# Kernel tuning notes

Hardware: AMD Instinct MI355X
Metric: run time of the kernel (lower is better)

Reference implementation:

```python
import jax, jax.numpy as jnp
import numpy as np

B, T, N_EMBED, HEAD_SIZE = 8, 2048, 1024, 64


def setup_inputs() -> dict:
    key = jax.random.key(0)
    kx, kq, kk, kv = jax.random.split(key, 4)
    x = jax.random.normal(kx, (B, T, N_EMBED), dtype=jnp.float32)
    # nn.Linear(n_embed, head_size, bias=False) -> weight [head_size, n_embed];
    # we store the transposed [n_embed, head_size] so projection is x @ W.
    s = 1.0 / np.sqrt(N_EMBED)
    Wq = jax.random.normal(kq, (N_EMBED, HEAD_SIZE), dtype=jnp.float32) * s
    Wk = jax.random.normal(kk, (N_EMBED, HEAD_SIZE), dtype=jnp.float32) * s
    Wv = jax.random.normal(kv, (N_EMBED, HEAD_SIZE), dtype=jnp.float32) * s
    pad_mask = jnp.ones((B, T), dtype=jnp.int32)
    return {"x": x, "pad_mask": pad_mask, "Wq": Wq, "Wk": Wk, "Wv": Wv}


def reference(x, pad_mask, Wq, Wk, Wv):
    Bq, Tq, C = x.shape  # C == n_embed
    q = x @ Wq  # [B,T,H]
    k = x @ Wk  # self-attention path (enc_x is None)
    v = x @ Wv
    # NOTE: original divides by C**0.5 with C = n_embed, not head_size.
    scores = jnp.einsum("bth,bsh->bts", q, k) / jnp.sqrt(jnp.asarray(C, x.dtype))
    causal = jnp.tril(jnp.ones((Tq, Tq), dtype=bool))  # tril[:T,:T] != 0
    keep = causal[None, :, :] & (pad_mask[:, None, :] != 0)  # [B,T,T]
    scores = jnp.where(keep, scores, -jnp.inf)
    attn = jax.nn.softmax(scores, axis=-1)
    return jnp.einsum("bts,bsh->bth", attn, v)  # [B,T,head_size]
```

## Files before the change

kernel.cpp:

```cpp
#include <hip/hip_runtime.h>

#define DEV static __device__ __forceinline__

typedef float f32x4 __attribute__((ext_vector_type(4)));
typedef __bf16 bf16x8 __attribute__((ext_vector_type(8)));
typedef unsigned short u16x8 __attribute__((ext_vector_type(8)));

#define MFMA(a, b, c) __builtin_amdgcn_mfma_f32_16x16x32_bf16((a), (b), (c), 0, 0, 0)

#define TT 2048
#define CE 1024
#define HS 64

#define WBT_E 0
#define Q_E   196608
#define K_E   (Q_E + 1048576)
#define VT_E  (K_E + 1048576)

DEV unsigned short cvt_bf16(float f) {
    unsigned int u = __builtin_bit_cast(unsigned int, f);
    u += 0x7FFFu + ((u >> 16) & 1u);
    return (unsigned short)(u >> 16);
}

DEV bf16x8 ld_bf8(const unsigned short* p) {
    union { u16x8 u; bf16x8 b; } v;
    v.u = *(const u16x8*)p;
    return v.b;
}

__global__ __launch_bounds__(256) void wconv_kernel(
        const float* __restrict__ Wq, const float* __restrict__ Wk,
        const float* __restrict__ Wv, unsigned short* __restrict__ wbt) {
    __shared__ unsigned short Tr[64 * 72];
    const int blk = blockIdx.x;
    const int head = blk >> 4, kt = blk & 15;
    const int k0 = kt * 64;
    const float* W = (head == 0) ? Wq : ((head == 1) ? Wk : Wv);
    const float sc = (head == 0) ? 0.045084220027780106f : 1.0f;
    const int t = threadIdx.x;
    const int rrow = t >> 4, c4 = (t & 15) * 4;
    for (int i = 0; i < 4; ++i) {
        int krow = rrow + i * 16;
        f32x4 f = *(const f32x4*)(W + (size_t)(k0 + krow) * 64 + c4);
        Tr[(c4 + 0) * 72 + krow] = cvt_bf16(f[0] * sc);
        Tr[(c4 + 1) * 72 + krow] = cvt_bf16(f[1] * sc);
        Tr[(c4 + 2) * 72 + krow] = cvt_bf16(f[2] * sc);
        Tr[(c4 + 3) * 72 + krow] = cvt_bf16(f[3] * sc);
    }
    __syncthreads();
    const int n = t >> 2, off = (t & 3) * 16;
    u16x8 a0 = *(const u16x8*)&Tr[n * 72 + off];
    u16x8 a1 = *(const u16x8*)&Tr[n * 72 + off + 8];
    unsigned short* dst = wbt + head * 65536 + n * 1024 + k0 + off;
    *(u16x8*)dst = a0;
    *(u16x8*)(dst + 8) = a1;
}

__global__ __launch_bounds__(256) void proj_kernel(
        const float* __restrict__ x, const unsigned short* __restrict__ wbt,
        unsigned short* __restrict__ qws, unsigned short* __restrict__ kws,
        unsigned short* __restrict__ vtws) {
    __shared__ __align__(16) unsigned short As[2 * 32 * 72];
    __shared__ __align__(16) unsigned short Ws[2 * 192 * 72];

    const int t = threadIdx.x;
    const int lane = t & 63, w = t >> 6;
    const int quad = lane >> 4, c = lane & 15;
    const int t0 = blockIdx.x * 32;
    const int xrow = t >> 3, xc = (t & 7) * 8;

    f32x4 acc[2][3] = {};

    {
        f32x4 f0 = *(const f32x4*)(x + (size_t)(t0 + xrow) * CE + xc);
        f32x4 f1 = *(const f32x4*)(x + (size_t)(t0 + xrow) * CE + xc + 4);
        u16x8 pk;
        for (int j = 0; j < 4; ++j) { pk[j] = cvt_bf16(f0[j]); pk[4 + j] = cvt_bf16(f1[j]); }
        *(u16x8*)&As[xrow * 72 + xc] = pk;
        for (int i = 0; i < 6; ++i) {
            int id = t + 256 * i, n = id >> 3, cc = id & 7;
            *(u16x8*)&Ws[n * 72 + cc * 8] = *(const u16x8*)(wbt + n * 1024 + cc * 8);
        }
    }
    __syncthreads();

    for (int step = 0; step < 16; ++step) {
        const int pb = step & 1, nb = pb ^ 1;
        const int ksn = ((step + 1) & 15) * 64;
        f32x4 f0 = *(const f32x4*)(x + (size_t)(t0 + xrow) * CE + ksn + xc);
        f32x4 f1 = *(const f32x4*)(x + (size_t)(t0 + xrow) * CE + ksn + xc + 4);
        u16x8 wv[6];
        for (int i = 0; i < 6; ++i) {
            int id = t + 256 * i, n = id >> 3, cc = id & 7;
            wv[i] = *(const u16x8*)(wbt + n * 1024 + ksn + cc * 8);
        }
        for (int kk = 0; kk < 2; ++kk) {
            bf16x8 a0 = ld_bf8(&As[pb * 2304 + c * 72 + kk * 32 + quad * 8]);
            bf16x8 a1 = ld_bf8(&As[pb * 2304 + (16 + c) * 72 + kk * 32 + quad * 8]);
            for (int nt = 0; nt < 3; ++nt) {
                bf16x8 bb = ld_bf8(&Ws[pb * 13824 + (w * 48 + nt * 16 + c) * 72 + kk * 32 + quad * 8]);
                acc[0][nt] = MFMA(a0, bb, acc[0][nt]);
                acc[1][nt] = MFMA(a1, bb, acc[1][nt]);
            }
        }
        {
            u16x8 pk;
            for (int j = 0; j < 4; ++j) { pk[j] = cvt_bf16(f0[j]); pk[4 + j] = cvt_bf16(f1[j]); }
            *(u16x8*)&As[nb * 2304 + xrow * 72 + xc] = pk;
            for (int i = 0; i < 6; ++i) {
                int id = t + 256 * i, n = id >> 3, cc = id & 7;
                *(u16x8*)&Ws[nb * 13824 + n * 72 + cc * 8] = wv[i];
            }
        }
        __syncthreads();
    }

    unsigned short* TT2 = As;
    for (int mt = 0; mt < 2; ++mt)
        for (int nt = 0; nt < 3; ++nt) {
            f32x4 a = acc[mt][nt];
            int col = w * 48 + nt * 16 + c;
            for (int r = 0; r < 4; ++r) {
                int row = mt * 16 + quad * 4 + r;
                size_t tg = (size_t)(t0 + row);
                unsigned short hv = cvt_bf16(a[r]);
                if (col < 64)       qws[tg * HS + col] = hv;
                else if (col < 128) kws[tg * HS + col - 64] = hv;
                else                TT2[(col - 128) * 48 + row] = hv;
            }
        }
    __syncthreads();
    {
        int h = t >> 2, off = (t & 3) * 8;
        u16x8 v = *(const u16x8*)&TT2[h * 48 + off];
        int b = t0 >> 11, tl0 = t0 & 2047;
        *(u16x8*)(vtws + (size_t)(b * 64 + h) * TT + tl0 + off) = v;
    }
}

__global__ __launch_bounds__(256) void flash_kernel(
        const unsigned short* __restrict__ qws, const unsigned short* __restrict__ kws,
        const unsigned short* __restrict__ vtws, const int* __restrict__ pmask,
        float* __restrict__ out) {
    __shared__ __align__(16) unsigned short Ks[2 * 64 * 72];
    __shared__ __align__(16) unsigned short Vts[2 * 64 * 72];
    __shared__ int pms[2 * 64];

    const int t = threadIdx.x, blk = blockIdx.x;
    const int b = blk >> 5, qi = blk & 31;
    const int t0 = qi * 64;
    const int lane = t & 63, w = t >> 6;
    const int quad = lane >> 4, c = lane & 15;
    const float NEGINF = -__builtin_inff();

    const int krow0 = t >> 3, kcc = (t & 7) * 8;
    const int vrow0 = w * 16 + (lane >> 3), vcc = (lane & 7) * 8;

    bf16x8 qf[2];
    for (int kk = 0; kk < 2; ++kk)
        qf[kk] = ld_bf8(qws + (size_t)(b * TT + t0 + w * 16 + c) * HS + kk * 32 + quad * 8);

    u16x8 kr0 = *(const u16x8*)(kws + (size_t)(b * TT + krow0) * HS + kcc);
    u16x8 kr1 = *(const u16x8*)(kws + (size_t)(b * TT + krow0 + 32) * HS + kcc);
    u16x8 vr0 = *(const u16x8*)(vtws + (size_t)(b * 64 + vrow0) * TT + vcc);
    u16x8 vr1 = *(const u16x8*)(vtws + (size_t)(b * 64 + vrow0 + 8) * TT + vcc);
    int pr = (t < 64) ? pmask[b * TT + t] : 0;
    *(u16x8*)&Ks[krow0 * 72 + kcc] = kr0;
    *(u16x8*)&Ks[(krow0 + 32) * 72 + kcc] = kr1;
    *(u16x8*)&Vts[vrow0 * 72 + vcc] = vr0;
    *(u16x8*)&Vts[(vrow0 + 8) * 72 + vcc] = vr1;
    if (t < 64) pms[t] = pr;
    __syncthreads();

    f32x4 o[4] = {};
    float m_run[4], l_run[4];
    for (int r = 0; r < 4; ++r) { m_run[r] = NEGINF; l_run[r] = 0.0f; }

    for (int jj = 0; jj <= qi; ++jj) {
        const int pb = jj & 1, nb = pb ^ 1;
        const int jn = (jj < qi) ? jj + 1 : qi;
        kr0 = *(const u16x8*)(kws + (size_t)(b * TT + jn * 64 + krow0) * HS + kcc);
        kr1 = *(const u16x8*)(kws + (size_t)(b * TT + jn * 64 + krow0 + 32) * HS + kcc);
        vr0 = *(const u16x8*)(vtws + (size_t)(b * 64 + vrow0) * TT + jn * 64 + vcc);
        vr1 = *(const u16x8*)(vtws + (size_t)(b * 64 + vrow0 + 8) * TT + jn * 64 + vcc);
        pr = (t < 64) ? pmask[b * TT + jn * 64 + t] : 0;

        f32x4 s4[4] = {};
        for (int kk = 0; kk < 2; ++kk)
            for (int nt = 0; nt < 4; ++nt) {
                bf16x8 bb = ld_bf8(&Ks[pb * 4608 + (nt * 16 + c) * 72 + kk * 32 + quad * 8]);
                s4[nt] = MFMA(qf[kk], bb, s4[nt]);
            }

        int pm4[4];
        for (int nt = 0; nt < 4; ++nt) pm4[nt] = pms[pb * 64 + nt * 16 + c];
        if (jj == qi) {
            for (int nt = 0; nt < 4; ++nt) {
                int col = nt * 16 + c;
                for (int r = 0; r < 4; ++r) {
                    int rowl = w * 16 + quad * 4 + r;
                    if (pm4[nt] == 0 || col > rowl) s4[nt][r] = NEGINF;
                }
            }
        } else {
            for (int nt = 0; nt < 4; ++nt)
                if (pm4[nt] == 0)
                    for (int r = 0; r < 4; ++r) s4[nt][r] = NEGINF;
        }

        float al[4];
        for (int r = 0; r < 4; ++r) {
            float mx = fmaxf(fmaxf(s4[0][r], s4[1][r]), fmaxf(s4[2][r], s4[3][r]));
            mx = fmaxf(mx, __shfl_xor(mx, 1, 64));
            mx = fmaxf(mx, __shfl_xor(mx, 2, 64));
            mx = fmaxf(mx, __shfl_xor(mx, 4, 64));
            mx = fmaxf(mx, __shfl_xor(mx, 8, 64));
            float mnew = fmaxf(m_run[r], mx);
            al[r] = (mnew == NEGINF) ? 1.0f : exp2f(m_run[r] - mnew);
            m_run[r] = mnew;
        }
        for (int nt = 0; nt < 4; ++nt)
            for (int r = 0; r < 4; ++r)
                s4[nt][r] = (s4[nt][r] == NEGINF) ? 0.0f : exp2f(s4[nt][r] - m_run[r]);
        for (int r = 0; r < 4; ++r) {
            float rs = s4[0][r] + s4[1][r] + s4[2][r] + s4[3][r];
            rs += __shfl_xor(rs, 1, 64);
            rs += __shfl_xor(rs, 2, 64);
            rs += __shfl_xor(rs, 4, 64);
            rs += __shfl_xor(rs, 8, 64);
            l_run[r] = l_run[r] * al[r] + rs;
        }
        for (int nt = 0; nt < 4; ++nt)
            for (int r = 0; r < 4; ++r) o[nt][r] *= al[r];

        unsigned short* Psw = &Vts[nb * 4608 + (w * 16) * 72];
        for (int nt = 0; nt < 4; ++nt)
            for (int r = 0; r < 4; ++r)
                Psw[(quad * 4 + r) * 72 + nt * 16 + c] = cvt_bf16(s4[nt][r]);

        for (int kk = 0; kk < 2; ++kk) {
            bf16x8 pa = ld_bf8(&Psw[c * 72 + kk * 32 + quad * 8]);
            for (int ht = 0; ht < 4; ++ht) {
                bf16x8 vb = ld_bf8(&Vts[pb * 4608 + (ht * 16 + c) * 72 + kk * 32 + quad * 8]);
                o[ht] = MFMA(pa, vb, o[ht]);
            }
        }

        *(u16x8*)&Ks[nb * 4608 + krow0 * 72 + kcc] = kr0;
        *(u16x8*)&Ks[nb * 4608 + (krow0 + 32) * 72 + kcc] = kr1;
        *(u16x8*)&Vts[nb * 4608 + vrow0 * 72 + vcc] = vr0;
        *(u16x8*)&Vts[nb * 4608 + (vrow0 + 8) * 72 + vcc] = vr1;
        if (t < 64) pms[nb * 64 + t] = pr;
        __syncthreads();
    }

    float inv[4];
    for (int r = 0; r < 4; ++r) inv[r] = 1.0f / l_run[r];
    for (int nt = 0; nt < 4; ++nt)
        for (int r = 0; r < 4; ++r)
            out[(size_t)(b * TT + t0 + w * 16 + quad * 4 + r) * HS + nt * 16 + c] =
                o[nt][r] * inv[r];
}

extern "C" void kernel_launch(void* const* d_in, const int* in_sizes, int n_in,
                              void* d_out, int out_size, void* d_ws, size_t ws_size,
                              hipStream_t stream) {
    const float* x  = (const float*)d_in[0];
    const int* pm   = (const int*)d_in[1];
    const float* Wq = (const float*)d_in[2];
    const float* Wk = (const float*)d_in[3];
    const float* Wv = (const float*)d_in[4];
    float* out = (float*)d_out;

    unsigned short* wsu  = (unsigned short*)d_ws;
    unsigned short* wbt  = wsu + WBT_E;
    unsigned short* qws  = wsu + Q_E;
    unsigned short* kws  = wsu + K_E;
    unsigned short* vtws = wsu + VT_E;

    wconv_kernel<<<48, 256, 0, stream>>>(Wq, Wk, Wv, wbt);
    proj_kernel<<<512, 256, 0, stream>>>(x, wbt, qws, kws, vtws);
    flash_kernel<<<256, 256, 0, stream>>>(qws, kws, vtws, pm, out);
}
```

Measured before the change: 174.6 us.

## Split flash attention into single-wave KV-split blocks with combine pass

The attention kernel is rebuilt so that each 64-thread block handles 16 query rows over one of up to four 512-wide key/value segments. K and V fragments are loaded straight from global memory into registers, with no shared-memory staging and no block barriers. A new combine kernel merges the partial outputs, which are stored in bf16 together with their running max and sum, to fix the causal load imbalance and the low block count of the old 256-block grid. The projection kernel also drops its shared-memory weight tile and keeps the weight fragments in registers. In exchange there is an extra launch, workspace round-trips, bf16 rounding of the partial outputs, and uncoalesced direct global loads.

```diff
diff --git a/kernel.cpp b/kernel.cpp
--- a/kernel.cpp
+++ b/kernel.cpp
@@ -5,6 +5,7 @@
 typedef float f32x4 __attribute__((ext_vector_type(4)));
 typedef __bf16 bf16x8 __attribute__((ext_vector_type(8)));
 typedef unsigned short u16x8 __attribute__((ext_vector_type(8)));
+typedef unsigned short u16x4 __attribute__((ext_vector_type(4)));
 
 #define MFMA(a, b, c) __builtin_amdgcn_mfma_f32_16x16x32_bf16((a), (b), (c), 0, 0, 0)
 
@@ -16,6 +17,8 @@
 #define Q_E   196608
 #define K_E   (Q_E + 1048576)
 #define VT_E  (K_E + 1048576)
+#define PO_E  (VT_E + 1048576)
+#define PML_E (PO_E + 4194304)
 
 DEV unsigned short cvt_bf16(float f) {
     unsigned int u = __builtin_bit_cast(unsigned int, f);
@@ -23,9 +26,20 @@
     return (unsigned short)(u >> 16);
 }
 
+DEV float bf2f(unsigned short v) {
+    unsigned int u = ((unsigned int)v) << 16;
+    return __builtin_bit_cast(float, u);
+}
+
 DEV bf16x8 ld_bf8(const unsigned short* p) {
     union { u16x8 u; bf16x8 b; } v;
     v.u = *(const u16x8*)p;
+    return v.b;
+}
+
+DEV bf16x8 as_bf8(u16x8 u) {
+    union { u16x8 u; bf16x8 b; } v;
+    v.u = u;
     return v.b;
 }
 
@@ -62,7 +76,6 @@
         unsigned short* __restrict__ qws, unsigned short* __restrict__ kws,
         unsigned short* __restrict__ vtws) {
     __shared__ __align__(16) unsigned short As[2 * 32 * 72];
-    __shared__ __align__(16) unsigned short Ws[2 * 192 * 72];
 
     const int t = threadIdx.x;
     const int lane = t & 63, w = t >> 6;
@@ -70,7 +83,10 @@
     const int t0 = blockIdx.x * 32;
     const int xrow = t >> 3, xc = (t & 7) * 8;
 
+    const unsigned short* wbase = wbt + (size_t)(w * 48 + c) * 1024 + quad * 8;
+
     f32x4 acc[2][3] = {};
+    u16x8 wc[3][2], wn[3][2];
 
     {
         f32x4 f0 = *(const f32x4*)(x + (size_t)(t0 + xrow) * CE + xc);
@@ -78,10 +94,9 @@
         u16x8 pk;
         for (int j = 0; j < 4; ++j) { pk[j] = cvt_bf16(f0[j]); pk[4 + j] = cvt_bf16(f1[j]); }
         *(u16x8*)&As[xrow * 72 + xc] = pk;
-        for (int i = 0; i < 6; ++i) {
-            int id = t + 256 * i, n = id >> 3, cc = id & 7;
-            *(u16x8*)&Ws[n * 72 + cc * 8] = *(const u16x8*)(wbt + n * 1024 + cc * 8);
-        }
+        for (int nt = 0; nt < 3; ++nt)
+            for (int kk = 0; kk < 2; ++kk)
+                wc[nt][kk] = *(const u16x8*)(wbase + nt * 16384 + kk * 32);
     }
     __syncthreads();
 
@@ -90,16 +105,14 @@
         const int ksn = ((step + 1) & 15) * 64;
         f32x4 f0 = *(const f32x4*)(x + (size_t)(t0 + xrow) * CE + ksn + xc);
         f32x4 f1 = *(const f32x4*)(x + (size_t)(t0 + xrow) * CE + ksn + xc + 4);
-        u16x8 wv[6];
-        for (int i = 0; i < 6; ++i) {
-            int id = t + 256 * i, n = id >> 3, cc = id & 7;
-            wv[i] = *(const u16x8*)(wbt + n * 1024 + ksn + cc * 8);
-        }
+        for (int nt = 0; nt < 3; ++nt)
+            for (int kk = 0; kk < 2; ++kk)
+                wn[nt][kk] = *(const u16x8*)(wbase + nt * 16384 + ksn + kk * 32);
         for (int kk = 0; kk < 2; ++kk) {
             bf16x8 a0 = ld_bf8(&As[pb * 2304 + c * 72 + kk * 32 + quad * 8]);
             bf16x8 a1 = ld_bf8(&As[pb * 2304 + (16 + c) * 72 + kk * 32 + quad * 8]);
             for (int nt = 0; nt < 3; ++nt) {
-                bf16x8 bb = ld_bf8(&Ws[pb * 13824 + (w * 48 + nt * 16 + c) * 72 + kk * 32 + quad * 8]);
+                bf16x8 bb = as_bf8(wc[nt][kk]);
                 acc[0][nt] = MFMA(a0, bb, acc[0][nt]);
                 acc[1][nt] = MFMA(a1, bb, acc[1][nt]);
             }
@@ -108,11 +121,9 @@
             u16x8 pk;
             for (int j = 0; j < 4; ++j) { pk[j] = cvt_bf16(f0[j]); pk[4 + j] = cvt_bf16(f1[j]); }
             *(u16x8*)&As[nb * 2304 + xrow * 72 + xc] = pk;
-            for (int i = 0; i < 6; ++i) {
-                int id = t + 256 * i, n = id >> 3, cc = id & 7;
-                *(u16x8*)&Ws[nb * 13824 + n * 72 + cc * 8] = wv[i];
-            }
-        }
+        }
+        for (int nt = 0; nt < 3; ++nt)
+            for (int kk = 0; kk < 2; ++kk) wc[nt][kk] = wn[nt][kk];
         __syncthreads();
     }
 
@@ -139,79 +150,78 @@
     }
 }
 
-__global__ __launch_bounds__(256) void flash_kernel(
+__global__ __launch_bounds__(64) void flash_kernel(
         const unsigned short* __restrict__ qws, const unsigned short* __restrict__ kws,
         const unsigned short* __restrict__ vtws, const int* __restrict__ pmask,
-        float* __restrict__ out) {
-    __shared__ __align__(16) unsigned short Ks[2 * 64 * 72];
-    __shared__ __align__(16) unsigned short Vts[2 * 64 * 72];
-    __shared__ int pms[2 * 64];
-
-    const int t = threadIdx.x, blk = blockIdx.x;
-    const int b = blk >> 5, qi = blk & 31;
-    const int t0 = qi * 64;
-    const int lane = t & 63, w = t >> 6;
+        unsigned short* __restrict__ pO, float* __restrict__ pml) {
+    __shared__ __align__(16) unsigned short Ps[16 * 40];
+
+    const int blk = blockIdx.x;
+    const int sp = blk & 3, qt = (blk >> 2) & 127, b = blk >> 9;
+    const int ns = (qt >> 5) + 1;
+    if (sp >= ns) return;
+    const int kvlen = qt * 16 + 16;
+    const int kvs = sp * 512;
+    const int kve = (kvs + 512 < kvlen) ? kvs + 512 : kvlen;
+    const int nch = (kve - kvs + 31) >> 5;
+    const int lane = threadIdx.x;
     const int quad = lane >> 4, c = lane & 15;
     const float NEGINF = -__builtin_inff();
 
-    const int krow0 = t >> 3, kcc = (t & 7) * 8;
-    const int vrow0 = w * 16 + (lane >> 3), vcc = (lane & 7) * 8;
+    const unsigned short* kbase = kws + (size_t)(b * TT + c) * HS + quad * 8;
+    const unsigned short* vbase = vtws + (size_t)(b * 64 + c) * TT + quad * 8;
 
     bf16x8 qf[2];
     for (int kk = 0; kk < 2; ++kk)
-        qf[kk] = ld_bf8(qws + (size_t)(b * TT + t0 + w * 16 + c) * HS + kk * 32 + quad * 8);
-
-    u16x8 kr0 = *(const u16x8*)(kws + (size_t)(b * TT + krow0) * HS + kcc);
-    u16x8 kr1 = *(const u16x8*)(kws + (size_t)(b * TT + krow0 + 32) * HS + kcc);
-    u16x8 vr0 = *(const u16x8*)(vtws + (size_t)(b * 64 + vrow0) * TT + vcc);
-    u16x8 vr1 = *(const u16x8*)(vtws + (size_t)(b * 64 + vrow0 + 8) * TT + vcc);
-    int pr = (t < 64) ? pmask[b * TT + t] : 0;
-    *(u16x8*)&Ks[krow0 * 72 + kcc] = kr0;
-    *(u16x8*)&Ks[(krow0 + 32) * 72 + kcc] = kr1;
-    *(u16x8*)&Vts[vrow0 * 72 + vcc] = vr0;
-    *(u16x8*)&Vts[(vrow0 + 8) * 72 + vcc] = vr1;
-    if (t < 64) pms[t] = pr;
-    __syncthreads();
+        qf[kk] = ld_bf8(qws + (size_t)(b * TT + qt * 16 + c) * HS + kk * 32 + quad * 8);
+
+    u16x8 kc[2][2], vc[4], kn[2][2], vn[4];
+    int pmc[2], pmn[2];
+    for (int nt = 0; nt < 2; ++nt) {
+        for (int kk = 0; kk < 2; ++kk)
+            kc[nt][kk] = *(const u16x8*)(kbase + (size_t)(kvs + nt * 16) * HS + kk * 32);
+        pmc[nt] = pmask[b * TT + kvs + nt * 16 + c];
+    }
+    for (int ht = 0; ht < 4; ++ht)
+        vc[ht] = *(const u16x8*)(vbase + (size_t)(ht * 16) * TT + kvs);
 
     f32x4 o[4] = {};
     float m_run[4], l_run[4];
     for (int r = 0; r < 4; ++r) { m_run[r] = NEGINF; l_run[r] = 0.0f; }
 
-    for (int jj = 0; jj <= qi; ++jj) {
-        const int pb = jj & 1, nb = pb ^ 1;
-        const int jn = (jj < qi) ? jj + 1 : qi;
-        kr0 = *(const u16x8*)(kws + (size_t)(b * TT + jn * 64 + krow0) * HS + kcc);
-        kr1 = *(const u16x8*)(kws + (size_t)(b * TT + jn * 64 + krow0 + 32) * HS + kcc);
-        vr0 = *(const u16x8*)(vtws + (size_t)(b * 64 + vrow0) * TT + jn * 64 + vcc);
-        vr1 = *(const u16x8*)(vtws + (size_t)(b * 64 + vrow0 + 8) * TT + jn * 64 + vcc);
-        pr = (t < 64) ? pmask[b * TT + jn * 64 + t] : 0;
-
-        f32x4 s4[4] = {};
+    for (int ch = 0; ch < nch; ++ch) {
+        const int kv0 = kvs + ch * 32;
+        const int kvn = (ch + 1 < nch) ? kv0 + 32 : kv0;
+        for (int nt = 0; nt < 2; ++nt) {
+            for (int kk = 0; kk < 2; ++kk)
+                kn[nt][kk] = *(const u16x8*)(kbase + (size_t)(kvn + nt * 16) * HS + kk * 32);
+            pmn[nt] = pmask[b * TT + kvn + nt * 16 + c];
+        }
+        for (int ht = 0; ht < 4; ++ht)
+            vn[ht] = *(const u16x8*)(vbase + (size_t)(ht * 16) * TT + kvn);
+
+        f32x4 s4[2] = {};
         for (int kk = 0; kk < 2; ++kk)
-            for (int nt = 0; nt < 4; ++nt) {
-                bf16x8 bb = ld_bf8(&Ks[pb * 4608 + (nt * 16 + c) * 72 + kk * 32 + quad * 8]);
-                s4[nt] = MFMA(qf[kk], bb, s4[nt]);
-            }
-
-        int pm4[4];
-        for (int nt = 0; nt < 4; ++nt) pm4[nt] = pms[pb * 64 + nt * 16 + c];
-        if (jj == qi) {
-            for (int nt = 0; nt < 4; ++nt) {
-                int col = nt * 16 + c;
+            for (int nt = 0; nt < 2; ++nt)
+                s4[nt] = MFMA(qf[kk], as_bf8(kc[nt][kk]), s4[nt]);
+
+        if (sp == ns - 1 && ch == nch - 1) {
+            for (int nt = 0; nt < 2; ++nt) {
+                int col = kv0 + nt * 16 + c;
                 for (int r = 0; r < 4; ++r) {
-                    int rowl = w * 16 + quad * 4 + r;
-                    if (pm4[nt] == 0 || col > rowl) s4[nt][r] = NEGINF;
+                    int row = qt * 16 + quad * 4 + r;
+                    if (pmc[nt] == 0 || col > row) s4[nt][r] = NEGINF;
                 }
             }
         } else {
-            for (int nt = 0; nt < 4; ++nt)
-                if (pm4[nt] == 0)
+            for (int nt = 0; nt < 2; ++nt)
+                if (pmc[nt] == 0)
                     for (int r = 0; r < 4; ++r) s4[nt][r] = NEGINF;
         }
 
         float al[4];
         for (int r = 0; r < 4; ++r) {
-            float mx = fmaxf(fmaxf(s4[0][r], s4[1][r]), fmaxf(s4[2][r], s4[3][r]));
+            float mx = fmaxf(s4[0][r], s4[1][r]);
             mx = fmaxf(mx, __shfl_xor(mx, 1, 64));
             mx = fmaxf(mx, __shfl_xor(mx, 2, 64));
             mx = fmaxf(mx, __shfl_xor(mx, 4, 64));
@@ -220,47 +230,81 @@
             al[r] = (mnew == NEGINF) ? 1.0f : exp2f(m_run[r] - mnew);
             m_run[r] = mnew;
         }
-        for (int nt = 0; nt < 4; ++nt)
+        for (int nt = 0; nt < 2; ++nt)
             for (int r = 0; r < 4; ++r)
                 s4[nt][r] = (s4[nt][r] == NEGINF) ? 0.0f : exp2f(s4[nt][r] - m_run[r]);
         for (int r = 0; r < 4; ++r) {
-            float rs = s4[0][r] + s4[1][r] + s4[2][r] + s4[3][r];
+            float rs = s4[0][r] + s4[1][r];
             rs += __shfl_xor(rs, 1, 64);
             rs += __shfl_xor(rs, 2, 64);
             rs += __shfl_xor(rs, 4, 64);
             rs += __shfl_xor(rs, 8, 64);
             l_run[r] = l_run[r] * al[r] + rs;
         }
-        for (int nt = 0; nt < 4; ++nt)
-            for (int r = 0; r < 4; ++r) o[nt][r] *= al[r];
-
-        unsigned short* Psw = &Vts[nb * 4608 + (w * 16) * 72];
-        for (int nt = 0; nt < 4; ++nt)
+        for (int ht = 0; ht < 4; ++ht)
+            for (int r = 0; r < 4; ++r) o[ht][r] *= al[r];
+
+        for (int nt = 0; nt < 2; ++nt)
             for (int r = 0; r < 4; ++r)
-                Psw[(quad * 4 + r) * 72 + nt * 16 + c] = cvt_bf16(s4[nt][r]);
-
-        for (int kk = 0; kk < 2; ++kk) {
-            bf16x8 pa = ld_bf8(&Psw[c * 72 + kk * 32 + quad * 8]);
-            for (int ht = 0; ht < 4; ++ht) {
-                bf16x8 vb = ld_bf8(&Vts[pb * 4608 + (ht * 16 + c) * 72 + kk * 32 + quad * 8]);
-                o[ht] = MFMA(pa, vb, o[ht]);
-            }
-        }
-
-        *(u16x8*)&Ks[nb * 4608 + krow0 * 72 + kcc] = kr0;
-        *(u16x8*)&Ks[nb * 4608 + (krow0 + 32) * 72 + kcc] = kr1;
-        *(u16x8*)&Vts[nb * 4608 + vrow0 * 72 + vcc] = vr0;
-        *(u16x8*)&Vts[nb * 4608 + (vrow0 + 8) * 72 + vcc] = vr1;
-        if (t < 64) pms[nb * 64 + t] = pr;
-        __syncthreads();
-    }
-
-    float inv[4];
-    for (int r = 0; r < 4; ++r) inv[r] = 1.0f / l_run[r];
-    for (int nt = 0; nt < 4; ++nt)
-        for (int r = 0; r < 4; ++r)
-            out[(size_t)(b * TT + t0 + w * 16 + quad * 4 + r) * HS + nt * 16 + c] =
-                o[nt][r] * inv[r];
+                Ps[(quad * 4 + r) * 40 + nt * 16 + c] = cvt_bf16(s4[nt][r]);
+        bf16x8 pa = ld_bf8(&Ps[c * 40 + quad * 8]);
+
+        for (int ht = 0; ht < 4; ++ht)
+            o[ht] = MFMA(pa, as_bf8(vc[ht]), o[ht]);
+
+        for (int nt = 0; nt < 2; ++nt) {
+            for (int kk = 0; kk < 2; ++kk) kc[nt][kk] = kn[nt][kk];
+            pmc[nt] = pmn[nt];
+        }
+        for (int ht = 0; ht < 4; ++ht) vc[ht] = vn[ht];
+    }
+
+    const int slot = blk;
+    unsigned short* po = pO + (size_t)slot * 1024;
+    for (int ht = 0; ht < 4; ++ht) {
+        u16x4 pk;
+        for (int r = 0; r < 4; ++r) pk[r] = cvt_bf16(o[ht][r]);
+        *(u16x4*)(po + (ht * 16 + c) * 16 + quad * 4) = pk;
+    }
+    if (c == 0)
+        for (int r = 0; r < 4; ++r) {
+            pml[(size_t)slot * 32 + (quad * 4 + r) * 2] = m_run[r];
+            pml[(size_t)slot * 32 + (quad * 4 + r) * 2 + 1] = l_run[r];
+        }
+}
+
+__global__ __launch_bounds__(256) void combine_kernel(
+        const unsigned short* __restrict__ pO, const float* __restrict__ pml,
+        float* __restrict__ out) {
+    const int blk = blockIdx.x;
+    const int b = blk >> 7, qt = blk & 127;
+    const int ns = (qt >> 5) + 1;
+    const int base = blk * 4;
+    const int t = threadIdx.x;
+    const int rowg = t >> 6, h = t & 63;
+
+    float msp[4][4], lsp[4][4];
+    for (int sp = 0; sp < ns; ++sp)
+        for (int r = 0; r < 4; ++r) {
+            msp[sp][r] = pml[(size_t)(base + sp) * 32 + (rowg * 4 + r) * 2];
+            lsp[sp][r] = pml[(size_t)(base + sp) * 32 + (rowg * 4 + r) * 2 + 1];
+        }
+    float M[4];
+    for (int r = 0; r < 4; ++r) {
+        M[r] = msp[0][r];
+        for (int sp = 1; sp < ns; ++sp) M[r] = fmaxf(M[r], msp[sp][r]);
+    }
+    float acc[4] = {}, den[4] = {};
+    for (int sp = 0; sp < ns; ++sp) {
+        u16x4 ov = *(const u16x4*)(pO + (size_t)(base + sp) * 1024 + h * 16 + rowg * 4);
+        for (int r = 0; r < 4; ++r) {
+            float wgt = exp2f(msp[sp][r] - M[r]);
+            den[r] += lsp[sp][r] * wgt;
+            acc[r] += bf2f(ov[r]) * wgt;
+        }
+    }
+    for (int r = 0; r < 4; ++r)
+        out[(size_t)(b * TT + qt * 16 + rowg * 4 + r) * HS + h] = acc[r] / den[r];
 }
 
 extern "C" void kernel_launch(void* const* d_in, const int* in_sizes, int n_in,
@@ -278,8 +322,11 @@
     unsigned short* qws  = wsu + Q_E;
     unsigned short* kws  = wsu + K_E;
     unsigned short* vtws = wsu + VT_E;
+    unsigned short* pO   = wsu + PO_E;
+    float* pml           = (float*)(wsu + PML_E);
 
     wconv_kernel<<<48, 256, 0, stream>>>(Wq, Wk, Wv, wbt);
     proj_kernel<<<512, 256, 0, stream>>>(x, wbt, qws, kws, vtws);
-    flash_kernel<<<256, 256, 0, stream>>>(qws, kws, vtws, pm, out);
-}
+    flash_kernel<<<4096, 64, 0, stream>>>(qws, kws, vtws, pm, pO, pml);
+    combine_kernel<<<1024, 256, 0, stream>>>(pO, pml, out);
+}
```

New measurement: 197.5 us. 1.13x slower.
